# Kernel optimization log

Hardware: AMD Instinct MI355X
Metric: run time of the kernel (lower is better)

Reference implementation:

```python
import jax, jax.numpy as jnp
import numpy as np

NUM_HEADS = 8
H_DIM = 24
COORDS_DIM = 3
NUM_W_PER_DIST = 8
BLOCK_SIZE = 128
N_HASHES = 3
N = 32768
HASH_DIM = H_DIM + (COORDS_DIM - 1) + 2  # q/k augmented with RPE coordinate terms


def layernorm(x, g, b, eps=1e-5):
    mu = x.mean(-1, keepdims=True)
    var = ((x - mu) ** 2).mean(-1, keepdims=True)
    return (x - mu) * jax.lax.rsqrt(var + eps) * g + b


def setup_inputs() -> dict:
    key = jax.random.key(0)
    ks = jax.random.split(key, 16)
    d, H = H_DIM, NUM_HEADS
    s = lambda i, shape, scale: jax.random.normal(ks[i], shape, jnp.float32) * scale
    return {
        "x": s(0, (N, d), 1.0),
        "coords": jax.random.uniform(ks[1], (N, COORDS_DIM), jnp.float32),
        "norm1_g": jnp.ones((d,), jnp.float32),
        "norm1_b": jnp.zeros((d,), jnp.float32),
        "Wq": s(2, (d, H * d), d ** -0.5),
        "Wk": s(3, (d, H * d), d ** -0.5),
        "Wv": s(4, (d, H * d), d ** -0.5),
        "w_rpe_W": s(5, (H * d, (COORDS_DIM - 1) * NUM_W_PER_DIST), 0.3),
        "Wo": s(6, (H * d, d), (H * d) ** -0.5),
        "bo": jnp.zeros((d,), jnp.float32),
        "norm2_g": jnp.ones((d,), jnp.float32),
        "norm2_b": jnp.zeros((d,), jnp.float32),
        "ff_W1": s(7, (d, d), d ** -0.5),
        "ff_b1": jnp.zeros((d,), jnp.float32),
        "ff_W2": s(8, (d, d), d ** -0.5),
        "ff_b2": jnp.zeros((d,), jnp.float32),
        "alphas": s(9, (N_HASHES, H, HASH_DIM), 1.0),  # E2LSH projection vectors
    }


def hept_attention(q, k, v, coords, w_rpe_W, alphas):
    # q,k,v: [n, H*d]. HEPT: fold RPE exp(-w*||dp||^2) into augmented q/k, then
    # n_hashes rounds of LSH sort + block-local attention, combined by softmax
    # over each round's log-normalizer (Reformer-style).
    n = q.shape[0]
    H, d, B = NUM_HEADS, H_DIM, BLOCK_SIZE
    nb = n // B
    q = q.reshape(n, H, d).transpose(1, 0, 2) * (d ** -0.5)  # [H,n,d]
    k = k.reshape(n, H, d).transpose(1, 0, 2)
    v = v.reshape(n, H, d).transpose(1, 0, 2)
    # per-head non-negative distance weights from w_rpe (mixture collapsed)
    Wm = w_rpe_W.reshape(H, d, COORDS_DIM - 1, NUM_W_PER_DIST)
    w = jnp.mean(Wm, axis=(1, 3)) ** 2                        # [H, c-1]
    p = coords[:, 1:]                                          # [n, c-1]
    sqn = jnp.einsum("hc,nc,nc->hn", w, p, p)                # w*||p||^2
    qp = jnp.sqrt(2.0) * jnp.sqrt(w)[:, None, :] * p[None]     # [H,n,c-1]
    ones = jnp.ones((H, n, 1), q.dtype)
    # q_hat.k_hat = q.k + 2*w*p_i.p_j - w|p_i|^2 - w|p_j|^2 = q.k - w*||p_i-p_j||^2
    q_hat = jnp.concatenate([q, qp, -sqn[..., None], ones], -1)  # [H,n,HASH_DIM]
    k_hat = jnp.concatenate([k, qp, ones, -sqn[..., None]], -1)
    outs, zs = [], []
    for r in range(N_HASHES):
        a = alphas[r]                                          # [H, HASH_DIM]
        iq = jnp.argsort(jnp.einsum("hne,he->hn", q_hat, a), -1)
        ik = jnp.argsort(jnp.einsum("hne,he->hn", k_hat, a), -1)
        qs = jnp.take_along_axis(q_hat, iq[..., None], 1).reshape(H, nb, B, -1)
        ks = jnp.take_along_axis(k_hat, ik[..., None], 1).reshape(H, nb, B, -1)
        vs = jnp.take_along_axis(v, ik[..., None], 1).reshape(H, nb, B, d)
        logits = jnp.einsum("hbqe,hbke->hbqk", qs, ks)         # [H,nb,B,B]
        z = jax.nn.logsumexp(logits, -1).reshape(H, n)
        o = jnp.einsum("hbqk,hbkd->hbqd", jax.nn.softmax(logits, -1), vs).reshape(H, n, d)
        inv = jnp.argsort(iq, -1)                              # unsort to input order
        outs.append(jnp.take_along_axis(o, inv[..., None], 1))
        zs.append(jnp.take_along_axis(z, inv, 1))
    wts = jax.nn.softmax(jnp.stack(zs), axis=0)[..., None]     # [R,H,n,1]
    out = (jnp.stack(outs) * wts).sum(0)                       # [H,n,d]
    return out.transpose(1, 0, 2).reshape(n, H * d)


def reference(x, coords, norm1_g, norm1_b, Wq, Wk, Wv, w_rpe_W, Wo, bo,
              norm2_g, norm2_b, ff_W1, ff_b1, ff_W2, ff_b2, alphas):
    xn = layernorm(x, norm1_g, norm1_b)
    q, k, v = xn @ Wq, xn @ Wk, xn @ Wv
    aggr = hept_attention(q, k, v, coords, w_rpe_W, alphas) @ Wo + bo
    x = x + aggr  # dropout is identity in eval mode
    h = layernorm(x, norm2_g, norm2_b)
    ff = jax.nn.relu(h @ ff_W1 + ff_b1) @ ff_W2 + ff_b2
    return x + ff
```

## Files before the change

kernel.cpp:

```cpp
#include <hip/hip_runtime.h>
#include <math.h>

#define NPT 32768
#define NH 8
#define HD 24
#define EDIM 28
#define NHASH 3
#define NSEG 48
#define NRH 24

typedef unsigned long long u64;
typedef unsigned short ushort;
typedef __attribute__((__vector_size__(8 * sizeof(short)))) short bf16x8;
typedef __attribute__((__vector_size__(4 * sizeof(float)))) float floatx4;

__device__ __forceinline__ ushort f2bf(float f) {
    unsigned u = __float_as_uint(f);
    unsigned r = u + 0x7FFF + ((u >> 16) & 1);
    return (ushort)(r >> 16);
}
__device__ __forceinline__ float us2f(ushort u) {
    return __uint_as_float(((unsigned)u) << 16);
}

__global__ __launch_bounds__(256) void k0b(
    const float* __restrict__ wrpe, const float* __restrict__ Wq,
    const float* __restrict__ Wk, const float* __restrict__ alphas,
    double* __restrict__ w64, double* __restrict__ cqp64,
    double* __restrict__ Aq, double* __restrict__ Ak, double* __restrict__ ct) {
    __shared__ double sw[16], sc[16];
    int t = threadIdx.x;
    if (t < 16) {
        int h = t >> 1, c = t & 1;
        double s = 0.0;
        for (int i = 0; i < 24; i++)
            for (int j = 0; j < 8; j++)
                s += (double)wrpe[(h * 24 + i) * 16 + c * 8 + j];
        double m = s / 192.0;
        sw[t] = m * m;
        sc[t] = sqrt(2.0) * fabs(m);
        w64[t] = sw[t];
        cqp64[t] = sc[t];
    }
    __syncthreads();
    const double QSCALE = 1.0 / sqrt(24.0);
    for (int idx = t; idx < 24 * NRH; idx += 256) {
        int i = idx / NRH, rh = idx % NRH;
        int h = rh & 7;
        double aq = 0.0, ak = 0.0;
        for (int e = 0; e < 24; e++) {
            double al = (double)alphas[rh * 28 + e];
            aq += (double)Wq[i * 192 + h * 24 + e] * al;
            ak += (double)Wk[i * 192 + h * 24 + e] * al;
        }
        Aq[idx] = aq * QSCALE;
        Ak[idx] = ak;
    }
    if (t < NRH) {
        int h = t & 7;
        ct[t * 4 + 0] = (double)alphas[t * 28 + 24] * sc[h * 2 + 0];
        ct[t * 4 + 1] = (double)alphas[t * 28 + 25] * sc[h * 2 + 1];
        ct[t * 4 + 2] = (double)alphas[t * 28 + 26];
        ct[t * 4 + 3] = (double)alphas[t * 28 + 27];
    }
}

__global__ __launch_bounds__(512) void k2s(
    const float* __restrict__ x, const float* __restrict__ n1g,
    const float* __restrict__ n1b, const float* __restrict__ coords,
    const double* __restrict__ Aq, const double* __restrict__ Ak,
    const double* __restrict__ ct, const double* __restrict__ w64,
    u64* __restrict__ keys, float* __restrict__ xnf) {
    __shared__ double sA[2][24][NRH];
    __shared__ double sCt[NRH][4];
    __shared__ double sW64[16];
    __shared__ double sGB[48];
    __shared__ double sXn[8][24];
    int t = threadIdx.x;
    for (int i = t; i < 24 * NRH; i += 512) sA[0][i / NRH][i % NRH] = Aq[i];
    for (int i = t; i < 24 * NRH; i += 512) sA[1][i / NRH][i % NRH] = Ak[i];
    for (int i = t; i < NRH * 4; i += 512) sCt[i / 4][i % 4] = ct[i];
    if (t < 16) sW64[t] = w64[t];
    if (t < 24) { sGB[t] = (double)n1g[t]; sGB[24 + t] = (double)n1b[t]; }
    __syncthreads();
    int wv = t >> 6, l = t & 63;
    for (int g = 0; g < 8; g++) {
        int n = blockIdx.x * 64 + g * 8 + wv;
        double xv = (l < 24) ? (double)x[(u64)n * 24 + l] : 0.0;
        double s = xv;
        s += __shfl_xor(s, 1); s += __shfl_xor(s, 2); s += __shfl_xor(s, 4);
        s += __shfl_xor(s, 8); s += __shfl_xor(s, 16);
        double mu = s / 24.0;
        double d = (l < 24) ? (xv - mu) : 0.0;
        double v2 = d * d;
        v2 += __shfl_xor(v2, 1); v2 += __shfl_xor(v2, 2); v2 += __shfl_xor(v2, 4);
        v2 += __shfl_xor(v2, 8); v2 += __shfl_xor(v2, 16);
        double rstd = 1.0 / sqrt(v2 / 24.0 + 1e-5);
        if (l < 24) {
            double xn = d * rstd * sGB[l] + sGB[24 + l];
            sXn[wv][l] = xn;
            xnf[(u64)n * 24 + l] = (float)xn;
        }
        double p0 = (double)coords[(u64)n * 3 + 1];
        double p1 = (double)coords[(u64)n * 3 + 2];
        if (l < 2 * NRH) {
            int qk = l / NRH, rh = l % NRH;
            int h = rh & 7;
            double sqn = sW64[2 * h] * p0 * p0 + sW64[2 * h + 1] * p1 * p1;
            double acc = sCt[rh][0] * p0 + sCt[rh][1] * p1;
            acc += qk ? (sCt[rh][2] - sqn * sCt[rh][3]) : (sCt[rh][3] - sqn * sCt[rh][2]);
            for (int i = 0; i < 24; i++) acc += sXn[wv][i] * sA[qk][i][rh];
            u64 u = (u64)__double_as_longlong(acc);
            if (u >> 63) u = ~u; else u |= 0x8000000000000000ULL;
            u64 key = (u & ~(u64)32767) | (u64)n;
            keys[(u64)l * NPT + n] = key;
        }
    }
}

#define K2P_PTS 64
__global__ __launch_bounds__(640) void k2p(
    const float* __restrict__ xnf,
    const float* __restrict__ Wq, const float* __restrict__ Wk,
    const float* __restrict__ Wv, const float* __restrict__ coords,
    const double* __restrict__ w64, const double* __restrict__ cqp64,
    ushort* __restrict__ qhatB, ushort* __restrict__ khatB, ushort* __restrict__ varrB) {
    int t = threadIdx.x;
    int n0 = blockIdx.x * K2P_PTS;
    if (t < 576) {
        int m = t / 192, jj = t % 192;
        const float* W = (m == 0) ? Wq : ((m == 1) ? Wk : Wv);
        float wc[24];
#pragma unroll
        for (int i = 0; i < 24; i++) wc[i] = W[i * 192 + jj];
        const float scale = (m == 0) ? (float)(1.0 / sqrt(24.0)) : 1.0f;
        int h = jj / 24, e = jj % 24;
        ushort* outp = (m == 0) ? qhatB : ((m == 1) ? khatB : varrB);
        ushort* obase = outp + (u64)h * NPT * 32 + e;
        for (int p = 0; p < K2P_PTS; p++) {
            int n = n0 + p;
            const float* xr = xnf + (u64)n * 24;
            float acc = 0.f;
#pragma unroll
            for (int i = 0; i < 24; i++) acc += xr[i] * wc[i];
            obase[(u64)n * 32] = f2bf(acc * scale);
        }
    } else {
        int l = t - 576;
        int h2 = l >> 3, e2 = 24 + (l & 7);
        double c0 = cqp64[h2 * 2], c1 = cqp64[h2 * 2 + 1];
        double wa = w64[h2 * 2], wb = w64[h2 * 2 + 1];
        ushort* qb = qhatB + (u64)h2 * NPT * 32 + e2;
        ushort* kb = khatB + (u64)h2 * NPT * 32 + e2;
        for (int p = 0; p < K2P_PTS; p++) {
            int n = n0 + p;
            double p0 = (double)coords[(u64)n * 3 + 1];
            double p1 = (double)coords[(u64)n * 3 + 2];
            float qv, kv;
            if (e2 < 26) {
                int c = e2 - 24;
                float qp = (float)((c ? c1 : c0) * (c ? p1 : p0));
                qv = qp; kv = qp;
            } else if (e2 < 28) {
                double sqn = wa * p0 * p0 + wb * p1 * p1;
                if (e2 == 26) { qv = (float)(-sqn); kv = 1.0f; }
                else          { qv = 1.0f; kv = (float)(-sqn); }
            } else {
                qv = 0.0f; kv = 0.0f;
            }
            qb[(u64)n * 32] = f2bf(qv);
            kb[(u64)n * 32] = f2bf(kv);
        }
    }
}

__device__ __forceinline__ u64 shflx64(u64 v, int d) {
    int lo = __shfl_xor((int)(unsigned)v, d);
    int hi = __shfl_xor((int)(unsigned)(v >> 32), d);
    return ((u64)(unsigned)hi << 32) | (unsigned)lo;
}
__device__ __forceinline__ void cswap(u64& a, u64& b, bool up) {
    if ((a > b) == up) { u64 tmp = a; a = b; b = tmp; }
}
__device__ __forceinline__ u64* sslot(u64* s, int i) {
    int a = i << 3;
    a ^= ((a >> 9) & 7) << 4;
    return (u64*)((char*)s + a);
}
__device__ __forceinline__ void reg_passes(u64 e[8], int ib, int K, int jmax) {
    for (int j = jmax; j >= 1; j >>= 1) {
#pragma unroll
        for (int k = 0; k < 8; k++)
            if ((k & j) == 0) cswap(e[k], e[k | j], ((ib + k) & K) == 0);
    }
}
__device__ __forceinline__ void shfl_passes(u64 e[8], int t, int segoff, int K, int jhi, int jlo) {
    for (int j = jhi; j >= jlo; j >>= 1) {
        int d = j >> 3;
        bool lower = (t & d) == 0;
        bool up = ((segoff + ((t & ~d) << 3)) & K) == 0;
        bool keepmin = (lower == up);
#pragma unroll
        for (int k = 0; k < 8; k++) {
            u64 o = shflx64(e[k], d);
            bool ownsm = e[k] < o;
            e[k] = (ownsm == keepmin) ? e[k] : o;
        }
    }
}

__global__ __launch_bounds__(1024) void sort_local_full(u64* keys) {
    __shared__ u64 s[8192];
    int t = threadIdx.x;
    u64 gbase = (u64)blockIdx.x * 8192;
    int segoff = (int)(gbase & 32767);
    int ib = segoff + t * 8;
    u64 e[8];
#pragma unroll
    for (int k = 0; k < 8; k++) e[k] = keys[gbase + t * 8 + k];
    reg_passes(e, ib, 2, 1);
    reg_passes(e, ib, 4, 2);
    reg_passes(e, ib, 8, 4);
    for (int K = 16; K <= 512; K <<= 1) {
        shfl_passes(e, t, segoff, K, K >> 1, 8);
        reg_passes(e, ib, K, 4);
    }
#pragma unroll
    for (int k = 0; k < 8; k++) *sslot(s, t * 8 + k) = e[k];
    __syncthreads();
    for (int K = 1024; K <= 8192; K <<= 1) {
        for (int j = K >> 1; j >= 512; j >>= 1) {
            for (int p = t; p < 4096; p += 1024) {
                int i = ((p & ~(j - 1)) << 1) | (p & (j - 1));
                int i2 = i | j;
                bool up = (((segoff + i) & K) == 0);
                u64 a = *sslot(s, i), b = *sslot(s, i2);
                if ((a > b) == up) { *sslot(s, i) = b; *sslot(s, i2) = a; }
            }
            __syncthreads();
        }
#pragma unroll
        for (int k = 0; k < 8; k++) e[k] = *sslot(s, t * 8 + k);
        shfl_passes(e, t, segoff, K, 256, 8);
        reg_passes(e, ib, K, 4);
        if (K < 8192) {
#pragma unroll
            for (int k = 0; k < 8; k++) *sslot(s, t * 8 + k) = e[k];
            __syncthreads();
        } else {
#pragma unroll
            for (int k = 0; k < 8; k++) keys[gbase + t * 8 + k] = e[k];
        }
    }
}

__global__ __launch_bounds__(1024) void sort_tail1_fused(u64* keys) {
    __shared__ u64 s[8192];
    int t = threadIdx.x;
    u64 gbase = (u64)blockIdx.x * 8192;
    u64 pbase = gbase ^ 8192ULL;
    int ci = (int)((gbase >> 13) & 3);
    bool keepmin = (ci == 0) || (ci == 3);
    int segoff = (int)(gbase & 32767);
    int ib = segoff + t * 8;
    for (int i = t; i < 8192; i += 1024) {
        u64 a = keys[gbase + i];
        u64 b = keys[pbase + i];
        u64 mn = a < b ? a : b;
        u64 mx = a < b ? b : a;
        *sslot(s, i) = keepmin ? mn : mx;
    }
    __syncthreads();
    const int K = 16384;
    for (int j = 4096; j >= 512; j >>= 1) {
        for (int p = t; p < 4096; p += 1024) {
            int i = ((p & ~(j - 1)) << 1) | (p & (j - 1));
            int i2 = i | j;
            bool up = (((segoff + i) & K) == 0);
            u64 a = *sslot(s, i), b = *sslot(s, i2);
            if ((a > b) == up) { *sslot(s, i) = b; *sslot(s, i2) = a; }
        }
        __syncthreads();
    }
    u64 e[8];
#pragma unroll
    for (int k = 0; k < 8; k++) e[k] = *sslot(s, t * 8 + k);
    shfl_passes(e, t, segoff, K, 256, 8);
    reg_passes(e, ib, K, 4);
#pragma unroll
    for (int k = 0; k < 8; k++) keys[gbase + t * 8 + k] = e[k];
}

__global__ __launch_bounds__(1024) void sort_local_tail(u64* keys, int K, int minj) {
    __shared__ u64 s[8192];
    int t = threadIdx.x;
    u64 gbase = (u64)blockIdx.x * 8192;
    int segoff = (int)(gbase & 32767);
    int ib = segoff + t * 8;
    for (int i = t; i < 8192; i += 1024) *sslot(s, i) = keys[gbase + i];
    __syncthreads();
    for (int j = 4096; j >= 512; j >>= 1) {
        for (int p = t; p < 4096; p += 1024) {
            int i = ((p & ~(j - 1)) << 1) | (p & (j - 1));
            int i2 = i | j;
            bool up = (((segoff + i) & K) == 0);
            u64 a = *sslot(s, i), b = *sslot(s, i2);
            if ((a > b) == up) { *sslot(s, i) = b; *sslot(s, i2) = a; }
        }
        __syncthreads();
    }
    u64 e[8];
#pragma unroll
    for (int k = 0; k < 8; k++) e[k] = *sslot(s, t * 8 + k);
    shfl_passes(e, t, segoff, K, 256, minj >= 8 ? minj : 8);
    if (minj < 8) reg_passes(e, ib, K, 4);
#pragma unroll
    for (int k = 0; k < 8; k++) keys[gbase + t * 8 + k] = e[k];
}

__global__ void sort_global2(u64* keys) {
    int p = blockIdx.x * blockDim.x + threadIdx.x;
    if (p >= NSEG * 8192) return;
    int seg = p >> 13, c = p & 8191;
    u64 base = (u64)seg * 32768 + c;
    u64 e0 = keys[base];
    u64 e1 = keys[base + 8192];
    u64 e2 = keys[base + 16384];
    u64 e3 = keys[base + 24576];
    u64 tmp;
    if (e0 > e2) { tmp = e0; e0 = e2; e2 = tmp; }
    if (e1 > e3) { tmp = e1; e1 = e3; e3 = tmp; }
    if (e0 > e1) { tmp = e0; e0 = e1; e1 = tmp; }
    if (e2 > e3) { tmp = e2; e2 = e3; e3 = tmp; }
    keys[base] = e0;
    keys[base + 8192] = e1;
    keys[base + 16384] = e2;
    keys[base + 24576] = e3;
}

#define VT_STRIDE 136
#define P_STRIDE 72
__global__ __launch_bounds__(256, 4) void k3_attn(
    const u64* __restrict__ keys, const ushort* __restrict__ qhatB,
    const ushort* __restrict__ khatB, const ushort* __restrict__ varrB,
    ushort* __restrict__ ozB) {
    int rh3 = blockIdx.x % 24;
    int b = blockIdx.x / 24;
    int h = rh3 & 7, r = rh3 >> 3;
    __shared__ __align__(16) char smem[6528 + 18432 + 1024];
    short* sVt = (short*)smem;
    short* sP  = (short*)(smem + 6528);
    int* qidx  = (int*)(smem + 6528 + 18432);
    int* kidx  = qidx + 128;
    int t = threadIdx.x;
    int segQ = r * 8 + h, segK = 24 + r * 8 + h;
    if (t < 128) {
        qidx[t] = (int)(keys[(u64)segQ * NPT + b * 128 + t] & 32767ULL);
    } else {
        int i = t - 128;
        kidx[i] = (int)(keys[(u64)segK * NPT + b * 128 + i] & 32767ULL);
    }
    __syncthreads();

    int wave = t >> 6, L = t & 63;
    int quad = L >> 4, n16 = L & 15;

    const bf16x8* Qg = (const bf16x8*)(qhatB + (u64)h * NPT * 32);
    const bf16x8* Kg = (const bf16x8*)(khatB + (u64)h * NPT * 32);
    bf16x8 afr[2];
#pragma unroll
    for (int rtg = 0; rtg < 2; rtg++) {
        int qi = qidx[wave * 32 + rtg * 16 + n16];
        afr[rtg] = Qg[(u64)qi * 4 + quad];
    }
    bf16x8 bfr[8];
#pragma unroll
    for (int ct = 0; ct < 8; ct++) {
        int ki = kidx[ct * 16 + n16];
        bfr[ct] = Kg[(u64)ki * 4 + quad];
    }
    if (t < 128) {
        int ki = kidx[t];
        const bf16x8* vr = (const bf16x8*)(varrB + ((u64)h * NPT + ki) * 32);
        bf16x8 v0 = vr[0], v1 = vr[1], v2 = vr[2];
#pragma unroll
        for (int e = 0; e < 8; e++) {
            sVt[e * VT_STRIDE + t]        = v0[e];
            sVt[(8 + e) * VT_STRIDE + t]  = v1[e];
            sVt[(16 + e) * VT_STRIDE + t] = v2[e];
        }
    }
    __syncthreads();

    floatx4 acc[2][8];
#pragma unroll
    for (int rtg = 0; rtg < 2; rtg++)
#pragma unroll
        for (int ct = 0; ct < 8; ct++)
            acc[rtg][ct] = (floatx4){0.f, 0.f, 0.f, 0.f};
#pragma unroll
    for (int ct = 0; ct < 8; ct++) {
#pragma unroll
        for (int rtg = 0; rtg < 2; rtg++)
            acc[rtg][ct] = __builtin_amdgcn_mfma_f32_16x16x32_bf16(afr[rtg], bfr[ct], acc[rtg][ct], 0, 0, 0);
    }

    float mrow[2][4], srow[2][4];
#pragma unroll
    for (int rtg = 0; rtg < 2; rtg++) {
#pragma unroll
        for (int rg = 0; rg < 4; rg++) {
            float m = -1e30f;
#pragma unroll
            for (int ct = 0; ct < 8; ct++) m = fmaxf(m, acc[rtg][ct][rg]);
            m = fmaxf(m, __shfl_xor(m, 1));
            m = fmaxf(m, __shfl_xor(m, 2));
            m = fmaxf(m, __shfl_xor(m, 4));
            m = fmaxf(m, __shfl_xor(m, 8));
            mrow[rtg][rg] = m;
            float s = 0.0f;
            int row = wave * 32 + rtg * 16 + quad * 4 + rg;
#pragma unroll
            for (int ct = 0; ct < 8; ct++) {
                float p = __expf(acc[rtg][ct][rg] - m);
                s += p;
                if (ct < 4) sP[row * P_STRIDE + ct * 16 + n16] = (short)f2bf(p);
            }
            s += __shfl_xor(s, 1);
            s += __shfl_xor(s, 2);
            s += __shfl_xor(s, 4);
            s += __shfl_xor(s, 8);
            srow[rtg][rg] = s;
        }
    }

    floatx4 occ[2][2];
#pragma unroll
    for (int rtg = 0; rtg < 2; rtg++)
#pragma unroll
        for (int ct2 = 0; ct2 < 2; ct2++)
            occ[rtg][ct2] = (floatx4){0.f, 0.f, 0.f, 0.f};
#pragma unroll
    for (int ks = 0; ks < 2; ks++) {
        bf16x8 bv[2], av[2];
#pragma unroll
        for (int ct2 = 0; ct2 < 2; ct2++)
            bv[ct2] = *(const bf16x8*)(sVt + (ct2 * 16 + n16) * VT_STRIDE + ks * 32 + quad * 8);
#pragma unroll
        for (int rtg = 0; rtg < 2; rtg++)
            av[rtg] = *(const bf16x8*)(sP + (wave * 32 + rtg * 16 + n16) * P_STRIDE + ks * 32 + quad * 8);
#pragma unroll
        for (int rtg = 0; rtg < 2; rtg++)
#pragma unroll
            for (int ct2 = 0; ct2 < 2; ct2++)
                occ[rtg][ct2] = __builtin_amdgcn_mfma_f32_16x16x32_bf16(av[rtg], bv[ct2], occ[rtg][ct2], 0, 0, 0);
    }
#pragma unroll
    for (int rtg = 0; rtg < 2; rtg++) {
#pragma unroll
        for (int rg = 0; rg < 4; rg++) {
            int row = wave * 32 + rtg * 16 + quad * 4 + rg;
#pragma unroll
            for (int ct = 4; ct < 8; ct++) {
                float p = __expf(acc[rtg][ct][rg] - mrow[rtg][rg]);
                sP[row * P_STRIDE + (ct - 4) * 16 + n16] = (short)f2bf(p);
            }
        }
    }
#pragma unroll
    for (int ks = 2; ks < 4; ks++) {
        bf16x8 bv[2], av[2];
#pragma unroll
        for (int ct2 = 0; ct2 < 2; ct2++)
            bv[ct2] = *(const bf16x8*)(sVt + (ct2 * 16 + n16) * VT_STRIDE + ks * 32 + quad * 8);
#pragma unroll
        for (int rtg = 0; rtg < 2; rtg++)
            av[rtg] = *(const bf16x8*)(sP + (wave * 32 + rtg * 16 + n16) * P_STRIDE + (ks - 2) * 32 + quad * 8);
#pragma unroll
        for (int rtg = 0; rtg < 2; rtg++)
#pragma unroll
            for (int ct2 = 0; ct2 < 2; ct2++)
                occ[rtg][ct2] = __builtin_amdgcn_mfma_f32_16x16x32_bf16(av[rtg], bv[ct2], occ[rtg][ct2], 0, 0, 0);
    }

#pragma unroll
    for (int rtg = 0; rtg < 2; rtg++) {
#pragma unroll
        for (int rg = 0; rg < 4; rg++) {
            int row = wave * 32 + rtg * 16 + quad * 4 + rg;
            int oi = qidx[row];
            float inv = 1.0f / srow[rtg][rg];
            ushort* orow = ozB + ((u64)segQ * NPT + oi) * 32;
#pragma unroll
            for (int ct2 = 0; ct2 < 2; ct2++) {
                int col = ct2 * 16 + n16;
                if (col < 24) orow[col] = f2bf(occ[rtg][ct2][rg] * inv);
            }
            if (n16 == 0)
                *(float*)(orow + 24) = mrow[rtg][rg] + __logf(srow[rtg][rg]);
        }
    }
}

#define K4PTS 32
#define AT_STR 196
#define W_STR 28
__global__ __launch_bounds__(256) void k4_final(
    const ushort* __restrict__ ozB,
    const float* __restrict__ x,
    const float* __restrict__ Wo, const float* __restrict__ bo,
    const float* __restrict__ g2, const float* __restrict__ b2,
    const float* __restrict__ W1, const float* __restrict__ b1f,
    const float* __restrict__ W2, const float* __restrict__ b2f,
    float* __restrict__ out) {
    __shared__ __align__(16) float sWoT[24][AT_STR];
    __shared__ __align__(16) float sW1T[24][W_STR], sW2T[24][W_STR];
    __shared__ float sB[5 * 24];
    __shared__ __align__(16) float attn[K4PTS][AT_STR];
    __shared__ float xrow[K4PTS][25];
    __shared__ __align__(16) float h2row[K4PTS][W_STR];
    __shared__ __align__(16) float ffrow[K4PTS][W_STR];
    int t = threadIdx.x;
    int base = blockIdx.x * K4PTS;
    for (int i = t; i < 4608; i += 256) sWoT[i % 24][i / 24] = Wo[i];
    for (int i = t; i < 576; i += 256) {
        sW1T[i % 24][i / 24] = W1[i];
        sW2T[i % 24][i / 24] = W2[i];
    }
    if (t < 24) {
        sB[t] = bo[t]; sB[24 + t] = g2[t]; sB[48 + t] = b2[t];
        sB[72 + t] = b1f[t]; sB[96 + t] = b2f[t];
    }
    if (t < K4PTS * 4) {
        int p = t >> 2, c = 24 + (t & 3);
        h2row[p][c] = 0.f; ffrow[p][c] = 0.f;
    }
    if (t < 24 * 4) {
        int rr = t >> 2, c = 24 + (t & 3);
        sW1T[rr][c] = 0.f; sW2T[rr][c] = 0.f;
    }
    {
        int p = t >> 3, h = t & 7;
        int n = base + p;
        const ushort* r0 = ozB + ((u64)(0 * 8 + h) * NPT + n) * 32;
        const ushort* r1 = ozB + ((u64)(1 * 8 + h) * NPT + n) * 32;
        const ushort* r2 = ozB + ((u64)(2 * 8 + h) * NPT + n) * 32;
        float z0 = *(const float*)(r0 + 24);
        float z1 = *(const float*)(r1 + 24);
        float z2 = *(const float*)(r2 + 24);
        float zm = fmaxf(z0, fmaxf(z1, z2));
        float e0 = __expf(z0 - zm), e1 = __expf(z1 - zm), e2 = __expf(z2 - zm);
        float inv = 1.0f / (e0 + e1 + e2);
        float w0 = e0 * inv, w1 = e1 * inv, w2 = e2 * inv;
#pragma unroll
        for (int e = 0; e < 24; e++)
            attn[p][h * 24 + e] = w0 * us2f(r0[e]) + w1 * us2f(r1[e]) + w2 * us2f(r2[e]);
    }
    __syncthreads();
    int p = t >> 3, oe = t & 7;
    int n = base + p;
    {
        const floatx4* ap = (const floatx4*)&attn[p][0];
        const floatx4* w0p = (const floatx4*)&sWoT[oe][0];
        const floatx4* w1p = (const floatx4*)&sWoT[oe + 8][0];
        const floatx4* w2p = (const floatx4*)&sWoT[oe + 16][0];
        floatx4 A0 = {0.f, 0.f, 0.f, 0.f}, A1 = A0, A2 = A0;
        for (int ii = 0; ii < 48; ii++) {
            floatx4 av = ap[ii];
            A0 += av * w0p[ii];
            A1 += av * w1p[ii];
            A2 += av * w2p[ii];
        }
        float a0 = A0[0] + A0[1] + A0[2] + A0[3];
        float a1 = A1[0] + A1[1] + A1[2] + A1[3];
        float a2 = A2[0] + A2[1] + A2[2] + A2[3];
        xrow[p][oe]      = x[n * 24 + oe]      + a0 + sB[oe];
        xrow[p][oe + 8]  = x[n * 24 + oe + 8]  + a1 + sB[oe + 8];
        xrow[p][oe + 16] = x[n * 24 + oe + 16] + a2 + sB[oe + 16];
    }
    float mu, rstd;
    {
        float s = xrow[p][oe] + xrow[p][oe + 8] + xrow[p][oe + 16];
        s += __shfl_xor(s, 1); s += __shfl_xor(s, 2); s += __shfl_xor(s, 4);
        mu = s / 24.0f;
        float v0 = xrow[p][oe] - mu, v1 = xrow[p][oe + 8] - mu, v2 = xrow[p][oe + 16] - mu;
        float v = v0 * v0 + v1 * v1 + v2 * v2;
        v += __shfl_xor(v, 1); v += __shfl_xor(v, 2); v += __shfl_xor(v, 4);
        rstd = 1.0f / sqrtf(v / 24.0f + 1e-5f);
    }
    h2row[p][oe]      = (xrow[p][oe] - mu)      * rstd * sB[24 + oe]      + sB[48 + oe];
    h2row[p][oe + 8]  = (xrow[p][oe + 8] - mu)  * rstd * sB[24 + oe + 8]  + sB[48 + oe + 8];
    h2row[p][oe + 16] = (xrow[p][oe + 16] - mu) * rstd * sB[24 + oe + 16] + sB[48 + oe + 16];
    {
        const floatx4* hp = (const floatx4*)&h2row[p][0];
        const floatx4* w0p = (const floatx4*)&sW1T[oe][0];
        const floatx4* w1p = (const floatx4*)&sW1T[oe + 8][0];
        const floatx4* w2p = (const floatx4*)&sW1T[oe + 16][0];
        floatx4 A0 = {0.f, 0.f, 0.f, 0.f}, A1 = A0, A2 = A0;
#pragma unroll
        for (int ii = 0; ii < 6; ii++) {
            floatx4 hv = hp[ii];
            A0 += hv * w0p[ii];
            A1 += hv * w1p[ii];
            A2 += hv * w2p[ii];
        }
        ffrow[p][oe]      = fmaxf(A0[0]+A0[1]+A0[2]+A0[3] + sB[72 + oe], 0.f);
        ffrow[p][oe + 8]  = fmaxf(A1[0]+A1[1]+A1[2]+A1[3] + sB[72 + oe + 8], 0.f);
        ffrow[p][oe + 16] = fmaxf(A2[0]+A2[1]+A2[2]+A2[3] + sB[72 + oe + 16], 0.f);
    }
    {
        const floatx4* fp = (const floatx4*)&ffrow[p][0];
        const floatx4* w0p = (const floatx4*)&sW2T[oe][0];
        const floatx4* w1p = (const floatx4*)&sW2T[oe + 8][0];
        const floatx4* w2p = (const floatx4*)&sW2T[oe + 16][0];
        floatx4 A0 = {0.f, 0.f, 0.f, 0.f}, A1 = A0, A2 = A0;
#pragma unroll
        for (int ii = 0; ii < 6; ii++) {
            floatx4 fv = fp[ii];
            A0 += fv * w0p[ii];
            A1 += fv * w1p[ii];
            A2 += fv * w2p[ii];
        }
        out[n * 24 + oe]      = xrow[p][oe]      + A0[0]+A0[1]+A0[2]+A0[3] + sB[96 + oe];
        out[n * 24 + oe + 8]  = xrow[p][oe + 8]  + A1[0]+A1[1]+A1[2]+A1[3] + sB[96 + oe + 8];
        out[n * 24 + oe + 16] = xrow[p][oe + 16] + A2[0]+A2[1]+A2[2]+A2[3] + sB[96 + oe + 16];
    }
}

extern "C" void kernel_launch(void* const* d_in, const int* in_sizes, int n_in,
                              void* d_out, int out_size, void* d_ws, size_t ws_size,
                              hipStream_t stream) {
    const float* x      = (const float*)d_in[0];
    const float* coords = (const float*)d_in[1];
    const float* n1g    = (const float*)d_in[2];
    const float* n1b    = (const float*)d_in[3];
    const float* Wq     = (const float*)d_in[4];
    const float* Wk     = (const float*)d_in[5];
    const float* Wv     = (const float*)d_in[6];
    const float* wrpe   = (const float*)d_in[7];
    const float* Wo     = (const float*)d_in[8];
    const float* bo     = (const float*)d_in[9];
    const float* n2g    = (const float*)d_in[10];
    const float* n2b    = (const float*)d_in[11];
    const float* W1     = (const float*)d_in[12];
    const float* b1     = (const float*)d_in[13];
    const float* W2     = (const float*)d_in[14];
    const float* b2     = (const float*)d_in[15];
    const float* alphas = (const float*)d_in[16];

    char* ws = (char*)d_ws;
    size_t off = 0;
    auto alloc = [&](size_t bytes) -> void* {
        void* p = ws + off;
        off = (off + bytes + 255) & ~(size_t)255;
        return p;
    };
    double* w64   = (double*)alloc(256);
    double* cqp   = (double*)alloc(256);
    double* Aq    = (double*)alloc(24 * NRH * 8);
    double* Ak    = (double*)alloc(24 * NRH * 8);
    double* ct    = (double*)alloc(NRH * 4 * 8);
    float*  xnf   = (float*)alloc((size_t)NPT * 24 * 4);
    ushort* qhatB = (ushort*)alloc((size_t)NH * NPT * 32 * 2);
    ushort* khatB = (ushort*)alloc((size_t)NH * NPT * 32 * 2);
    ushort* varrB = (ushort*)alloc((size_t)NH * NPT * 32 * 2);
    u64*    keys  = (u64*)alloc((size_t)NSEG * NPT * 8);
    ushort* ozB   = (ushort*)alloc((size_t)NHASH * NH * NPT * 32 * 2);
    if (off > ws_size) return;

    k0b<<<1, 256, 0, stream>>>(wrpe, Wq, Wk, alphas, w64, cqp, Aq, Ak, ct);
    k2s<<<NPT / 64, 512, 0, stream>>>(x, n1g, n1b, coords, Aq, Ak, ct, w64, keys, xnf);
    k2p<<<NPT / K2P_PTS, 640, 0, stream>>>(xnf, Wq, Wk, Wv, coords, w64, cqp,
                                           qhatB, khatB, varrB);
    sort_local_full<<<192, 1024, 0, stream>>>(keys);
    sort_tail1_fused<<<192, 1024, 0, stream>>>(keys);
    sort_global2<<<NSEG * 8192 / 256, 256, 0, stream>>>(keys);
    sort_local_tail<<<192, 1024, 0, stream>>>(keys, 32768, 128);
    k3_attn<<<256 * 8 * 3, 256, 0, stream>>>(keys, qhatB, khatB, varrB, ozB);
    k4_final<<<NPT / K4PTS, 256, 0, stream>>>(ozB, x, Wo, bo, n2g, n2b,
                                              W1, b1, W2, b2, (float*)d_out);
}
```

Before: 308.4 us.

## Store full P tile with XOR-swizzled LDS layout and packed bf16 conversion

Replaces the padded-stride sV/sP shared-memory layouts with 256-byte rows that use an XOR swizzle, and stores all eight probability columns at once. Keys are permuted within the row so a single 16-byte vector write covers them, with conversion done through v_cvt_pk_bf16_f32. This removes the second exp pass and the split P·V loop, and replaces scalar LDS stores and software bf16 rounding. The cost is a larger LDS footprint (about 39KB per block versus about 26KB), which may limit occupancy. It also relies on the key permutation matching between the sV write and the sP/sV reads.

```diff
diff --git a/kernel.cpp b/kernel.cpp
--- a/kernel.cpp
+++ b/kernel.cpp
@@ -13,6 +13,7 @@
 typedef unsigned short ushort;
 typedef __attribute__((__vector_size__(8 * sizeof(short)))) short bf16x8;
 typedef __attribute__((__vector_size__(4 * sizeof(float)))) float floatx4;
+typedef __attribute__((__vector_size__(4 * sizeof(unsigned int)))) unsigned int uint32x4;
 
 __device__ __forceinline__ ushort f2bf(float f) {
     unsigned u = __float_as_uint(f);
@@ -338,8 +339,6 @@
     keys[base + 24576] = e3;
 }
 
-#define VT_STRIDE 136
-#define P_STRIDE 72
 __global__ __launch_bounds__(256, 4) void k3_attn(
     const u64* __restrict__ keys, const ushort* __restrict__ qhatB,
     const ushort* __restrict__ khatB, const ushort* __restrict__ varrB,
@@ -347,18 +346,18 @@
     int rh3 = blockIdx.x % 24;
     int b = blockIdx.x / 24;
     int h = rh3 & 7, r = rh3 >> 3;
-    __shared__ __align__(16) char smem[6528 + 18432 + 1024];
-    short* sVt = (short*)smem;
-    short* sP  = (short*)(smem + 6528);
-    int* qidx  = (int*)(smem + 6528 + 18432);
-    int* kidx  = qidx + 128;
+    __shared__ __align__(16) char smem[6144 + 32768 + 512];
+    char* sVt = smem;
+    char* sP  = smem + 6144;
+    ushort* qidx = (ushort*)(smem + 6144 + 32768);
+    ushort* kidx = qidx + 128;
     int t = threadIdx.x;
     int segQ = r * 8 + h, segK = 24 + r * 8 + h;
     if (t < 128) {
-        qidx[t] = (int)(keys[(u64)segQ * NPT + b * 128 + t] & 32767ULL);
+        qidx[t] = (ushort)(keys[(u64)segQ * NPT + b * 128 + t] & 32767ULL);
     } else {
         int i = t - 128;
-        kidx[i] = (int)(keys[(u64)segK * NPT + b * 128 + i] & 32767ULL);
+        kidx[i] = (ushort)(keys[(u64)segK * NPT + b * 128 + i] & 32767ULL);
     }
     __syncthreads();
 
@@ -383,11 +382,13 @@
         int ki = kidx[t];
         const bf16x8* vr = (const bf16x8*)(varrB + ((u64)h * NPT + ki) * 32);
         bf16x8 v0 = vr[0], v1 = vr[1], v2 = vr[2];
+        int colb = ((t & 15) << 4) | ((t >> 4) << 1);
 #pragma unroll
         for (int e = 0; e < 8; e++) {
-            sVt[e * VT_STRIDE + t]        = v0[e];
-            sVt[(8 + e) * VT_STRIDE + t]  = v1[e];
-            sVt[(16 + e) * VT_STRIDE + t] = v2[e];
+            int e0 = e, e1 = 8 + e, e2 = 16 + e;
+            *(short*)(sVt + e0 * 256 + (colb ^ ((e0 & 7) << 4))) = v0[e];
+            *(short*)(sVt + e1 * 256 + (colb ^ ((e1 & 7) << 4))) = v1[e];
+            *(short*)(sVt + e2 * 256 + (colb ^ ((e2 & 7) << 4))) = v2[e];
         }
     }
     __syncthreads();
@@ -410,27 +411,34 @@
     for (int rtg = 0; rtg < 2; rtg++) {
 #pragma unroll
         for (int rg = 0; rg < 4; rg++) {
-            float m = -1e30f;
-#pragma unroll
-            for (int ct = 0; ct < 8; ct++) m = fmaxf(m, acc[rtg][ct][rg]);
+            float m = acc[rtg][0][rg];
+#pragma unroll
+            for (int ct = 1; ct < 8; ct++) m = fmaxf(m, acc[rtg][ct][rg]);
             m = fmaxf(m, __shfl_xor(m, 1));
             m = fmaxf(m, __shfl_xor(m, 2));
             m = fmaxf(m, __shfl_xor(m, 4));
             m = fmaxf(m, __shfl_xor(m, 8));
             mrow[rtg][rg] = m;
+            float p[8];
             float s = 0.0f;
-            int row = wave * 32 + rtg * 16 + quad * 4 + rg;
 #pragma unroll
             for (int ct = 0; ct < 8; ct++) {
-                float p = __expf(acc[rtg][ct][rg] - m);
-                s += p;
-                if (ct < 4) sP[row * P_STRIDE + ct * 16 + n16] = (short)f2bf(p);
+                p[ct] = __expf(acc[rtg][ct][rg] - m);
+                s += p[ct];
             }
             s += __shfl_xor(s, 1);
             s += __shfl_xor(s, 2);
             s += __shfl_xor(s, 4);
             s += __shfl_xor(s, 8);
             srow[rtg][rg] = s;
+            unsigned w0, w1, w2, w3;
+            asm("v_cvt_pk_bf16_f32 %0, %1, %2" : "=v"(w0) : "v"(p[0]), "v"(p[1]));
+            asm("v_cvt_pk_bf16_f32 %0, %1, %2" : "=v"(w1) : "v"(p[2]), "v"(p[3]));
+            asm("v_cvt_pk_bf16_f32 %0, %1, %2" : "=v"(w2) : "v"(p[4]), "v"(p[5]));
+            asm("v_cvt_pk_bf16_f32 %0, %1, %2" : "=v"(w3) : "v"(p[6]), "v"(p[7]));
+            int row = wave * 32 + rtg * 16 + quad * 4 + rg;
+            uint32x4 pk = {w0, w1, w2, w3};
+            *(uint32x4*)(sP + row * 256 + (((n16 << 4)) ^ ((row & 7) << 4))) = pk;
         }
     }
 
@@ -441,41 +449,20 @@
         for (int ct2 = 0; ct2 < 2; ct2++)
             occ[rtg][ct2] = (floatx4){0.f, 0.f, 0.f, 0.f};
 #pragma unroll
-    for (int ks = 0; ks < 2; ks++) {
+    for (int ks = 0; ks < 4; ks++) {
+        int kb = ks * 64 + quad * 16;
         bf16x8 bv[2], av[2];
 #pragma unroll
-        for (int ct2 = 0; ct2 < 2; ct2++)
-            bv[ct2] = *(const bf16x8*)(sVt + (ct2 * 16 + n16) * VT_STRIDE + ks * 32 + quad * 8);
-#pragma unroll
-        for (int rtg = 0; rtg < 2; rtg++)
-            av[rtg] = *(const bf16x8*)(sP + (wave * 32 + rtg * 16 + n16) * P_STRIDE + ks * 32 + quad * 8);
-#pragma unroll
-        for (int rtg = 0; rtg < 2; rtg++)
-#pragma unroll
-            for (int ct2 = 0; ct2 < 2; ct2++)
-                occ[rtg][ct2] = __builtin_amdgcn_mfma_f32_16x16x32_bf16(av[rtg], bv[ct2], occ[rtg][ct2], 0, 0, 0);
-    }
-#pragma unroll
-    for (int rtg = 0; rtg < 2; rtg++) {
-#pragma unroll
-        for (int rg = 0; rg < 4; rg++) {
-            int row = wave * 32 + rtg * 16 + quad * 4 + rg;
-#pragma unroll
-            for (int ct = 4; ct < 8; ct++) {
-                float p = __expf(acc[rtg][ct][rg] - mrow[rtg][rg]);
-                sP[row * P_STRIDE + (ct - 4) * 16 + n16] = (short)f2bf(p);
-            }
-        }
-    }
-#pragma unroll
-    for (int ks = 2; ks < 4; ks++) {
-        bf16x8 bv[2], av[2];
-#pragma unroll
-        for (int ct2 = 0; ct2 < 2; ct2++)
-            bv[ct2] = *(const bf16x8*)(sVt + (ct2 * 16 + n16) * VT_STRIDE + ks * 32 + quad * 8);
-#pragma unroll
-        for (int rtg = 0; rtg < 2; rtg++)
-            av[rtg] = *(const bf16x8*)(sP + (wave * 32 + rtg * 16 + n16) * P_STRIDE + (ks - 2) * 32 + quad * 8);
+        for (int ct2 = 0; ct2 < 2; ct2++) {
+            int e = ct2 * 16 + n16;
+            int ec = (e < 24) ? e : 0;
+            bv[ct2] = *(const bf16x8*)(sVt + ec * 256 + (kb ^ ((ec & 7) << 4)));
+        }
+#pragma unroll
+        for (int rtg = 0; rtg < 2; rtg++) {
+            int rowA = wave * 32 + rtg * 16 + n16;
+            av[rtg] = *(const bf16x8*)(sP + rowA * 256 + (kb ^ ((rowA & 7) << 4)));
+        }
 #pragma unroll
         for (int rtg = 0; rtg < 2; rtg++)
 #pragma unroll
```

Result: no change. 306.5 us (-0.6%).
